# Performance work log

Measured on AMD Instinct MI355X. Metric: run time of the kernel, lower is better.

## Reference

```python
import jax, jax.numpy as jnp
import numpy as np

B = 8192       # atmospheric columns (batch)
NLAY = 60      # vertical levels (RNN sequence length)
NX = 4         # per-level input features
NXS = 3        # surface scalar inputs
NH1 = 64       # rnn1 hidden
NH2 = 64       # rnn2 hidden
NMEM = 16      # latent memory width (nh_mem)
NY = 4         # per-level outputs
NYS = 3        # surface outputs


def _lstm(x, h0, c0, Wih, Whh, bih, bhh):
    """PyTorch-convention LSTM (gate order i,f,g,o). x: [B,T,nx] -> ([B,T,nh], hL, cL)."""
    b = bih + bhh
    WihT = Wih.T
    WhhT = Whh.T

    def step(carry, xt):
        h, c = carry
        g = xt @ WihT + h @ WhhT + b
        i, f, gg, o = jnp.split(g, 4, axis=-1)
        c = jax.nn.sigmoid(f) * c + jax.nn.sigmoid(i) * jnp.tanh(gg)
        h = jax.nn.sigmoid(o) * jnp.tanh(c)
        return (h, c), h

    (hL, cL), ys = jax.lax.scan(step, (h0, c0), jnp.swapaxes(x, 0, 1))
    return jnp.swapaxes(ys, 0, 1), hL, cL


def setup_inputs() -> dict:
    key = jax.random.key(0)
    ks = jax.random.split(key, 30)

    def p(i, shape):
        return jax.random.normal(ks[i], shape, jnp.float32) * 0.05

    return {
        "inputs_main": jax.random.normal(ks[0], (B, NLAY, NX), jnp.float32),
        "inputs_aux": jax.random.normal(ks[1], (B, NXS), jnp.float32),
        "rnn1_mem": jax.random.normal(ks[2], (B, NLAY, NMEM), jnp.float32),
        # mlp_initial: Linear(nx, nneur[0])
        "Wi": p(3, (NH1, NX)), "bi": p(4, (NH1,)),
        # mlp_surface1/2: Linear(nx_sfc, nh_rnn1)
        "Ws1": p(5, (NH1, NXS)), "bs1": p(6, (NH1,)),
        "Ws2": p(7, (NH1, NXS)), "bs2": p(8, (NH1,)),
        # mlp_toa1/2: Linear(1, nh_rnn2)
        "Wt1": p(9, (NH2, 1)), "bt1": p(10, (NH2,)),
        "Wt2": p(11, (NH2, 1)), "bt2": p(12, (NH2,)),
        # rnn1: LSTM(NH1+NMEM -> NH1)
        "Wih1": p(13, (4 * NH1, NH1 + NMEM)), "Whh1": p(14, (4 * NH1, NH1)),
        "bih1": p(15, (4 * NH1,)), "bhh1": p(16, (4 * NH1,)),
        # rnn2: LSTM(NH1 -> NH2)
        "Wih2": p(17, (4 * NH2, NH1)), "Whh2": p(18, (4 * NH2, NH2)),
        "bih2": p(19, (4 * NH2,)), "bhh2": p(20, (4 * NH2,)),
        # mlp_latent: Linear(NH2, NMEM)
        "Wl": p(21, (NMEM, NH2)), "bl": p(22, (NMEM,)),
        # mlp_output: Linear(NMEM, NY)
        "Wo": p(23, (NY, NMEM)), "bo": p(24, (NY,)),
        # mlp_surface_output: Linear(NH2, NYS)
        "Wso": p(25, (NYS, NH2)), "bso": p(26, (NYS,)),
    }


def reference(inputs_main, inputs_aux, rnn1_mem, Wi, bi, Ws1, bs1, Ws2, bs2,
              Wt1, bt1, Wt2, bt2, Wih1, Whh1, bih1, bhh1, Wih2, Whh2, bih2, bhh2,
              Wl, bl, Wo, bo, Wso, bso):
    # initial MLP + tanh
    x = jnp.tanh(inputs_main @ Wi.T + bi)                       # [B,L,NH1]
    # concat convective memory
    x = jnp.concatenate([x, rnn1_mem], axis=2)                  # [B,L,NH1+NMEM]
    # rnn1 runs surface->TOA: flip level axis
    x = jnp.flip(x, axis=1)
    hx = jnp.tanh(inputs_aux @ Ws1.T + bs1)                     # surface-conditioned h0
    cx = jnp.tanh(inputs_aux @ Ws2.T + bs2)
    r1, _, _ = _lstm(x, hx, cx, Wih1, Whh1, bih1, bhh1)
    r1 = jnp.flip(r1, axis=1)                                   # back to TOA->surface
    # rnn2 initialized from TOA scalar
    toa = inputs_aux[:, 1:2]
    hx2 = toa @ Wt1.T + bt1
    cx2 = toa @ Wt2.T + bt2
    r2, hL, _ = _lstm(r1, hx2, cx2, Wih2, Whh2, bih2, bhh2)     # [B,L,NH2]
    # intermediate latent MLP -> new per-level memory
    lat = r2 @ Wl.T + bl                                        # [B,L,NMEM]
    new_mem = lat
    out = lat @ Wo.T + bo                                       # [B,L,NY]
    out_sfc = hL @ Wso.T + bso                                  # [B,NYS]
    return (out, out_sfc, new_mem)
```

## Files before the change

kernel.cpp:

```cpp
#include <hip/hip_runtime.h>
#include <hip/hip_bf16.h>

#define BATCH 8192
#define NLAY  60
#define NH    64
#define ROWS  16
#define TPB   256
#define S1    168
#define S2    136

typedef unsigned short ushort_t;
typedef __attribute__((ext_vector_type(8))) short short8;
typedef __attribute__((ext_vector_type(4))) float f32x4;
typedef __attribute__((ext_vector_type(4))) float f4v;

__device__ __forceinline__ float rcp_(float x) { return __builtin_amdgcn_rcpf(x); }
__device__ __forceinline__ float sigm_(float x) { return rcp_(1.0f + __expf(-x)); }
__device__ __forceinline__ float tanh_(float x) { return 1.0f - 2.0f * rcp_(__expf(2.0f * x) + 1.0f); }
__device__ __forceinline__ ushort_t f2bu(float f) {
  unsigned u = __float_as_uint(f);
  return (ushort_t)((u + 0x7FFFu + ((u >> 16) & 1u)) >> 16);
}
__device__ __forceinline__ unsigned pkbf(float a, float b) {
  union { __hip_bfloat162 h; unsigned u; } c;
  c.h = __float22bfloat162_rn(make_float2(a, b));
  return c.u;
}
__device__ __forceinline__ f32x4 mfma16(short8 a, short8 b, f32x4 c) {
  return __builtin_amdgcn_mfma_f32_16x16x32_bf16(a, b, c, 0, 0, 0);
}

__global__ void wtranspose(const float* __restrict__ Wih1, const float* __restrict__ Whh1,
                           const float* __restrict__ Wih2, const float* __restrict__ Whh2,
                           const float* __restrict__ Wl,   const float* __restrict__ Wo,
                           const float* __restrict__ Wso,  ushort_t* __restrict__ frag) {
  int e = blockIdx.x * 256 + threadIdx.x;
  float v;
  if (e < 40960) {
    int j = e & 7, lx = (e >> 3) & 63, rest = e >> 9;
    int ks = rest % 5, gw = rest / 5;
    int g = gw & 3, wv = gw >> 2;
    int uu = wv * 16 + (lx & 15);
    int k = ks * 32 + (lx >> 4) * 8 + j;
    int row = g * 64 + uu;
    v = (k < 80) ? Wih1[row * 80 + k] : (k < 144 ? Whh1[row * 64 + (k - 80)] : 0.0f);
  } else if (e < 73728) {
    int e2 = e - 40960;
    int j = e2 & 7, lx = (e2 >> 3) & 63, rest = e2 >> 9;
    int ks = rest & 3, g = (rest >> 2) & 3, wv = rest >> 4;
    int uu = wv * 16 + (lx & 15);
    int k = ks * 32 + (lx >> 4) * 8 + j;
    int row = g * 64 + uu;
    v = (k < 64) ? Wih2[row * 64 + k] : Whh2[row * 64 + (k - 64)];
  } else if (e < 74752) {
    int e3 = e - 73728;
    int j = e3 & 7, lx = (e3 >> 3) & 63, ks = e3 >> 9;
    int n = lx & 15, k = ks * 32 + (lx >> 4) * 8 + j;
    v = Wl[n * 64 + k];
  } else if (e < 75776) {
    int e4 = e - 74752;
    int j = e4 & 7, lx = (e4 >> 3) & 63, ks = e4 >> 9;
    int n = lx & 15, k = ks * 32 + (lx >> 4) * 8 + j;
    v = 0.0f;
    if (n < 4) {
#pragma unroll
      for (int m = 0; m < 16; ++m) v += Wo[n * 16 + m] * Wl[m * 64 + k];
    }
  } else {
    int e5 = e - 75776;
    int j = e5 & 7, lx = (e5 >> 3) & 63, ks = e5 >> 9;
    int n = lx & 15, k = ks * 32 + (lx >> 4) * 8 + j;
    v = (n < 3) ? Wso[n * 64 + k] : 0.0f;
  }
  frag[e] = f2bu(v);
}

__global__ __launch_bounds__(TPB, 2)
void lstm_fused(const float* __restrict__ inputs_main, const float* __restrict__ inputs_aux,
                const float* __restrict__ rnn1_mem,
                const float* __restrict__ Wi,  const float* __restrict__ bi,
                const float* __restrict__ Ws1, const float* __restrict__ bs1,
                const float* __restrict__ Ws2, const float* __restrict__ bs2,
                const float* __restrict__ Wt1, const float* __restrict__ bt1,
                const float* __restrict__ Wt2, const float* __restrict__ bt2,
                const float* __restrict__ bih1, const float* __restrict__ bhh1,
                const float* __restrict__ bih2, const float* __restrict__ bhh2,
                const float* __restrict__ bl,  const float* __restrict__ Wo,
                const float* __restrict__ bo,  const float* __restrict__ bso,
                const ushort_t* __restrict__ frag,
                ushort_t* __restrict__ r1buf,
                float* __restrict__ out, float* __restrict__ out_sfc,
                float* __restrict__ new_mem) {
  const ushort_t* W1f = frag;
  const ushort_t* W2f = frag + 40960;
  const ushort_t* WlF = frag + 73728;
  const ushort_t* WcF = frag + 74752;
  const ushort_t* WsF = frag + 75776;

  __shared__ __align__(16) ushort_t xh1[2][16 * S1];
  __shared__ __align__(16) ushort_t xh2[2][16 * S2];
  __shared__ __align__(16) float inmS[16][244];

  const int tid = threadIdx.x;
  const int l  = tid & 63, w = tid >> 6;
  const int ln = l & 15,  lq = l >> 4;
  const int u  = w * 16 + ln;
  const int rowbase = lq * 4;
  const int b0 = blockIdx.x * ROWS;
  const int xr = tid >> 4, xm = tid & 15, xc0 = xm * 4;
  const int rr8 = tid >> 3, ch8 = tid & 7;

  short8 B1f[4][5];
#pragma unroll
  for (int g = 0; g < 4; ++g)
#pragma unroll
    for (int ks = 0; ks < 5; ++ks)
      B1f[g][ks] = *(const short8*)(W1f + (((w * 4 + g) * 5 + ks) << 9) + (l << 3));

  f4v wif[4];
#pragma unroll
  for (int cc = 0; cc < 4; ++cc) wif[cc] = *(const f4v*)(Wi + (xc0 + cc) * 4);
  f4v bifv = *(const f4v*)(bi + xc0);

  float bg1[4];
#pragma unroll
  for (int g = 0; g < 4; ++g) bg1[g] = bih1[g * 64 + u] + bhh1[g * 64 + u];

  for (int e = tid; e < 16 * 240; e += TPB) {
    int r = e / 240, c = e - r * 240;
    inmS[r][c] = inputs_main[(size_t)(b0 + r) * 240 + c];
  }
  {
    int r = tid >> 4, c = 144 + (tid & 15);
    xh1[0][r * S1 + c] = 0; xh1[1][r * S1 + c] = 0;
  }
  __syncthreads();

  float c1[4];
  {
    float mv = rnn1_mem[(size_t)(b0 + xr) * 960 + 59 * 16 + xm];
    xh1[0][xr * S1 + 64 + xm] = f2bu(mv);
    f4v xin = *(const f4v*)&inmS[xr][59 * 4];
    float xp[4];
#pragma unroll
    for (int cc = 0; cc < 4; ++cc)
      xp[cc] = tanh_(bifv[cc] + wif[cc][0]*xin[0] + wif[cc][1]*xin[1] + wif[cc][2]*xin[2] + wif[cc][3]*xin[3]);
    *(uint2*)&xh1[0][xr * S1 + xc0] = make_uint2(pkbf(xp[0], xp[1]), pkbf(xp[2], xp[3]));

    float w10 = Ws1[u * 3 + 0], w11 = Ws1[u * 3 + 1], w12 = Ws1[u * 3 + 2], bb1 = bs1[u];
    float w20 = Ws2[u * 3 + 0], w21 = Ws2[u * 3 + 1], w22 = Ws2[u * 3 + 2], bb2 = bs2[u];
#pragma unroll
    for (int reg = 0; reg < 4; ++reg) {
      int row = rowbase + reg;
      const float* ax = inputs_aux + (size_t)(b0 + row) * 3;
      float a0 = ax[0], a1 = ax[1], a2 = ax[2];
      xh1[0][row * S1 + 80 + u] = f2bu(tanh_(w10 * a0 + w11 * a1 + w12 * a2 + bb1));
      c1[reg] = tanh_(w20 * a0 + w21 * a1 + w22 * a2 + bb2);
    }
  }
  __syncthreads();

  int pb = 0;
  for (int t = NLAY - 1; t >= 0; --t) {
    const int nb = pb ^ 1;
    float mv = 0.0f; f4v xin = {};
    if (t > 0) {
      mv  = rnn1_mem[(size_t)(b0 + xr) * 960 + (t - 1) * 16 + xm];
      xin = *(const f4v*)&inmS[xr][(t - 1) * 4];
    }
    short8 af[5];
#pragma unroll
    for (int ks = 0; ks < 5; ++ks)
      af[ks] = *(const short8*)&xh1[pb][ln * S1 + ks * 32 + lq * 8];

    f32x4 acc[4];
#pragma unroll
    for (int g = 0; g < 4; ++g) acc[g] = (f32x4){bg1[g], bg1[g], bg1[g], bg1[g]};
#pragma unroll
    for (int ks = 0; ks < 5; ++ks)
#pragma unroll
      for (int g = 0; g < 4; ++g) acc[g] = mfma16(af[ks], B1f[g][ks], acc[g]);

    if (t > 0) {
      float xp[4];
#pragma unroll
      for (int cc = 0; cc < 4; ++cc)
        xp[cc] = tanh_(bifv[cc] + wif[cc][0]*xin[0] + wif[cc][1]*xin[1] + wif[cc][2]*xin[2] + wif[cc][3]*xin[3]);
      *(uint2*)&xh1[nb][xr * S1 + xc0] = make_uint2(pkbf(xp[0], xp[1]), pkbf(xp[2], xp[3]));
      xh1[nb][xr * S1 + 64 + xm] = f2bu(mv);
    }

    float h[4];
#pragma unroll
    for (int reg = 0; reg < 4; ++reg) {
      float ig = sigm_(acc[0][reg]);
      float fg = sigm_(acc[1][reg]);
      float gg = tanh_(acc[2][reg]);
      float og = sigm_(acc[3][reg]);
      float c  = fg * c1[reg] + ig * gg;
      c1[reg] = c;
      h[reg] = og * tanh_(c);
    }
    unsigned h01 = pkbf(h[0], h[1]), h23 = pkbf(h[2], h[3]);
    ushort_t hu[4] = {(ushort_t)h01, (ushort_t)(h01 >> 16), (ushort_t)h23, (ushort_t)(h23 >> 16)};
#pragma unroll
    for (int reg = 0; reg < 4; ++reg) {
      r1buf[((size_t)(b0 + rowbase + reg) * 60 + t) * 64 + u] = hu[reg];
      if (t > 0) xh1[nb][(rowbase + reg) * S1 + 80 + u] = hu[reg];
      else       xh2[0][(rowbase + reg) * S2 + u]       = hu[reg];
    }
    __syncthreads();
    pb = nb;
  }

  short8 B2f[4][4];
#pragma unroll
  for (int g = 0; g < 4; ++g)
#pragma unroll
    for (int ks = 0; ks < 4; ++ks)
      B2f[g][ks] = *(const short8*)(W2f + (((w * 4 + g) * 4 + ks) << 9) + (l << 3));
  float bg2[4];
#pragma unroll
  for (int g = 0; g < 4; ++g) bg2[g] = bih2[g * 64 + u] + bhh2[g * 64 + u];

  float c2[4];
  {
    float wt1u = Wt1[u], wt2u = Wt2[u], bt1u = bt1[u], bt2u = bt2[u];
#pragma unroll
    for (int reg = 0; reg < 4; ++reg) {
      int row = rowbase + reg;
      float toa = inputs_aux[(size_t)(b0 + row) * 3 + 1];
      xh2[0][row * S2 + 64 + u] = f2bu(toa * wt1u + bt1u);
      c2[reg] = toa * wt2u + bt2u;
    }
  }
  short8 PW0 = {}, PW1 = {};
  float pbias = 0.0f;
  if (w == 0) {
    PW0 = *(const short8*)(WlF + (l << 3));
    PW1 = *(const short8*)(WlF + 512 + (l << 3));
    pbias = bl[ln];
  } else if (w == 1) {
    PW0 = *(const short8*)(WcF + (l << 3));
    PW1 = *(const short8*)(WcF + 512 + (l << 3));
    if (ln < 4) {
      float a = bo[ln];
#pragma unroll
      for (int m = 0; m < 16; ++m) a += Wo[ln * 16 + m] * bl[m];
      pbias = a;
    }
  } else if (w == 2) {
    PW0 = *(const short8*)(WsF + (l << 3));
    PW1 = *(const short8*)(WsF + 512 + (l << 3));
    pbias = (ln < 3) ? bso[ln] : 0.0f;
  }
  __syncthreads();

  pb = 0;
  for (int t = 0; t < NLAY; ++t) {
    const int nb = pb ^ 1;
    short8 r1v = {};
    if (t < 59 && tid < 128)
      r1v = *(const short8*)(r1buf + ((size_t)(b0 + rr8) * 60 + (t + 1)) * 64 + ch8 * 8);
    short8 af2[4];
#pragma unroll
    for (int ks = 0; ks < 4; ++ks)
      af2[ks] = *(const short8*)&xh2[pb][ln * S2 + ks * 32 + lq * 8];

    f32x4 acc[4];
#pragma unroll
    for (int g = 0; g < 4; ++g) acc[g] = (f32x4){bg2[g], bg2[g], bg2[g], bg2[g]};
#pragma unroll
    for (int ks = 0; ks < 4; ++ks)
#pragma unroll
      for (int g = 0; g < 4; ++g) acc[g] = mfma16(af2[ks], B2f[g][ks], acc[g]);

    if (t > 0 && w < 2) {
      short8 aL0 = *(const short8*)&xh2[pb][ln * S2 + 64 + lq * 8];
      short8 aL1 = *(const short8*)&xh2[pb][ln * S2 + 96 + lq * 8];
      f32x4 ap = (f32x4){pbias, pbias, pbias, pbias};
      ap = mfma16(aL0, PW0, ap);
      ap = mfma16(aL1, PW1, ap);
      if (w == 0) {
#pragma unroll
        for (int reg = 0; reg < 4; ++reg)
          new_mem[((size_t)(b0 + rowbase + reg) * 60 + (t - 1)) * 16 + ln] = ap[reg];
      } else if (ln < 4) {
#pragma unroll
        for (int reg = 0; reg < 4; ++reg)
          out[((size_t)(b0 + rowbase + reg) * 60 + (t - 1)) * 4 + ln] = ap[reg];
      }
    }

    float h[4];
#pragma unroll
    for (int reg = 0; reg < 4; ++reg) {
      float ig = sigm_(acc[0][reg]);
      float fg = sigm_(acc[1][reg]);
      float gg = tanh_(acc[2][reg]);
      float og = sigm_(acc[3][reg]);
      float c  = fg * c2[reg] + ig * gg;
      c2[reg] = c;
      h[reg] = og * tanh_(c);
    }
    unsigned h01 = pkbf(h[0], h[1]), h23 = pkbf(h[2], h[3]);
    ushort_t hu[4] = {(ushort_t)h01, (ushort_t)(h01 >> 16), (ushort_t)h23, (ushort_t)(h23 >> 16)};
#pragma unroll
    for (int reg = 0; reg < 4; ++reg)
      xh2[nb][(rowbase + reg) * S2 + 64 + u] = hu[reg];
    if (t < 59 && tid < 128)
      *(short8*)&xh2[nb][rr8 * S2 + ch8 * 8] = r1v;
    __syncthreads();
    pb = nb;
  }

  if (w < 3) {
    short8 aL0 = *(const short8*)&xh2[0][ln * S2 + 64 + lq * 8];
    short8 aL1 = *(const short8*)&xh2[0][ln * S2 + 96 + lq * 8];
    f32x4 ap = (f32x4){pbias, pbias, pbias, pbias};
    ap = mfma16(aL0, PW0, ap);
    ap = mfma16(aL1, PW1, ap);
    if (w == 0) {
#pragma unroll
      for (int reg = 0; reg < 4; ++reg)
        new_mem[((size_t)(b0 + rowbase + reg) * 60 + 59) * 16 + ln] = ap[reg];
    } else if (w == 1) {
      if (ln < 4) {
#pragma unroll
        for (int reg = 0; reg < 4; ++reg)
          out[((size_t)(b0 + rowbase + reg) * 60 + 59) * 4 + ln] = ap[reg];
      }
    } else {
      if (ln < 3) {
#pragma unroll
        for (int reg = 0; reg < 4; ++reg)
          out_sfc[(size_t)(b0 + rowbase + reg) * 3 + ln] = ap[reg];
      }
    }
  }
}

extern "C" void kernel_launch(void* const* d_in, const int* in_sizes, int n_in,
                              void* d_out, int out_size, void* d_ws, size_t ws_size,
                              hipStream_t stream) {
  (void)in_sizes; (void)n_in; (void)out_size; (void)ws_size;
  const float* inputs_main = (const float*)d_in[0];
  const float* inputs_aux  = (const float*)d_in[1];
  const float* rnn1_mem    = (const float*)d_in[2];
  const float* Wi   = (const float*)d_in[3];
  const float* bi   = (const float*)d_in[4];
  const float* Ws1  = (const float*)d_in[5];
  const float* bs1  = (const float*)d_in[6];
  const float* Ws2  = (const float*)d_in[7];
  const float* bs2  = (const float*)d_in[8];
  const float* Wt1  = (const float*)d_in[9];
  const float* bt1  = (const float*)d_in[10];
  const float* Wt2  = (const float*)d_in[11];
  const float* bt2  = (const float*)d_in[12];
  const float* Wih1 = (const float*)d_in[13];
  const float* Whh1 = (const float*)d_in[14];
  const float* bih1 = (const float*)d_in[15];
  const float* bhh1 = (const float*)d_in[16];
  const float* Wih2 = (const float*)d_in[17];
  const float* Whh2 = (const float*)d_in[18];
  const float* bih2 = (const float*)d_in[19];
  const float* bhh2 = (const float*)d_in[20];
  const float* Wl   = (const float*)d_in[21];
  const float* bl   = (const float*)d_in[22];
  const float* Wo   = (const float*)d_in[23];
  const float* bo   = (const float*)d_in[24];
  const float* Wso  = (const float*)d_in[25];
  const float* bso  = (const float*)d_in[26];

  float* out     = (float*)d_out;
  float* out_sfc = out + (size_t)BATCH * NLAY * 4;
  float* new_mem = out_sfc + (size_t)BATCH * 3;

  ushort_t* frag  = (ushort_t*)d_ws;
  ushort_t* r1buf = (ushort_t*)((char*)d_ws + 153600);

  wtranspose<<<300, 256, 0, stream>>>(Wih1, Whh1, Wih2, Whh2, Wl, Wo, Wso, frag);
  lstm_fused<<<BATCH / ROWS, TPB, 0, stream>>>(
      inputs_main, inputs_aux, rnn1_mem, Wi, bi, Ws1, bs1, Ws2, bs2,
      Wt1, bt1, Wt2, bt2, bih1, bhh1, bih2, bhh2, bl, Wo, bo, bso,
      frag, r1buf, out, out_sfc, new_mem);
}
```

Baseline: 263.5 us.

## Split LSTM gates across 8 waves with shared-memory preactivation exchange

Doubles the block to 512 threads so each wave computes two of the four gate groups. Preactivations are exchanged through shared memory, and each lane then applies the nonlinearities for 2 rows × 1 unit. The memory input and inputs_main are preloaded into LDS as bf16 for the whole sequence, and the double-buffered xh arrays are replaced by single buffers with two barriers per step. The goal is more waves per CU and less per-step MFMA and register load per wave. In exchange it adds an extra barrier and an LDS round-trip on every recurrent step.

```diff
diff --git a/kernel.cpp b/kernel.cpp
--- a/kernel.cpp
+++ b/kernel.cpp
@@ -5,12 +5,15 @@
 #define NLAY  60
 #define NH    64
 #define ROWS  16
-#define TPB   256
-#define S1    168
-#define S2    136
+#define TPB   512
+#define SX    136
+#define SM    968
+#define SP    273
+#define SI    244
 
 typedef unsigned short ushort_t;
 typedef __attribute__((ext_vector_type(8))) short short8;
+typedef __attribute__((ext_vector_type(4))) short short4v;
 typedef __attribute__((ext_vector_type(4))) float f32x4;
 typedef __attribute__((ext_vector_type(4))) float f4v;
 
@@ -21,11 +24,7 @@
   unsigned u = __float_as_uint(f);
   return (ushort_t)((u + 0x7FFFu + ((u >> 16) & 1u)) >> 16);
 }
-__device__ __forceinline__ unsigned pkbf(float a, float b) {
-  union { __hip_bfloat162 h; unsigned u; } c;
-  c.h = __float22bfloat162_rn(make_float2(a, b));
-  return c.u;
-}
+__device__ __forceinline__ float b2fu(ushort_t b) { return __uint_as_float(((unsigned)b) << 16); }
 __device__ __forceinline__ f32x4 mfma16(short8 a, short8 b, f32x4 c) {
   return __builtin_amdgcn_mfma_f32_16x16x32_bf16(a, b, c, 0, 0, 0);
 }
@@ -40,17 +39,18 @@
     int j = e & 7, lx = (e >> 3) & 63, rest = e >> 9;
     int ks = rest % 5, gw = rest / 5;
     int g = gw & 3, wv = gw >> 2;
-    int uu = wv * 16 + (lx & 15);
+    int row = g * 64 + wv * 16 + (lx & 15);
     int k = ks * 32 + (lx >> 4) * 8 + j;
-    int row = g * 64 + uu;
-    v = (k < 80) ? Wih1[row * 80 + k] : (k < 144 ? Whh1[row * 64 + (k - 80)] : 0.0f);
+    v = (k < 64)  ? Wih1[row * 80 + k]
+      : (k < 128) ? Whh1[row * 64 + (k - 64)]
+      : (k < 144) ? Wih1[row * 80 + 64 + (k - 128)]
+      : 0.0f;
   } else if (e < 73728) {
     int e2 = e - 40960;
     int j = e2 & 7, lx = (e2 >> 3) & 63, rest = e2 >> 9;
     int ks = rest & 3, g = (rest >> 2) & 3, wv = rest >> 4;
-    int uu = wv * 16 + (lx & 15);
+    int row = g * 64 + wv * 16 + (lx & 15);
     int k = ks * 32 + (lx >> 4) * 8 + j;
-    int row = g * 64 + uu;
     v = (k < 64) ? Wih2[row * 64 + k] : Whh2[row * 64 + (k - 64)];
   } else if (e < 74752) {
     int e3 = e - 73728;
@@ -75,7 +75,7 @@
   frag[e] = f2bu(v);
 }
 
-__global__ __launch_bounds__(TPB, 2)
+__global__ __launch_bounds__(TPB, 4)
 void lstm_fused(const float* __restrict__ inputs_main, const float* __restrict__ inputs_aux,
                 const float* __restrict__ rnn1_mem,
                 const float* __restrict__ Wi,  const float* __restrict__ bi,
@@ -97,244 +97,276 @@
   const ushort_t* WcF = frag + 74752;
   const ushort_t* WsF = frag + 75776;
 
-  __shared__ __align__(16) ushort_t xh1[2][16 * S1];
-  __shared__ __align__(16) ushort_t xh2[2][16 * S2];
-  __shared__ __align__(16) float inmS[16][244];
-
-  const int tid = threadIdx.x;
-  const int l  = tid & 63, w = tid >> 6;
-  const int ln = l & 15,  lq = l >> 4;
-  const int u  = w * 16 + ln;
-  const int rowbase = lq * 4;
-  const int b0 = blockIdx.x * ROWS;
-  const int xr = tid >> 4, xm = tid & 15, xc0 = xm * 4;
-  const int rr8 = tid >> 3, ch8 = tid & 7;
-
-  short8 B1f[4][5];
-#pragma unroll
-  for (int g = 0; g < 4; ++g)
+  __shared__ __align__(16) ushort_t xh1[16 * SX];
+  __shared__ __align__(16) ushort_t xh2[16 * SX];
+  __shared__ __align__(16) ushort_t memAll[16 * SM];
+  __shared__ __align__(16) float    preactS[16 * SP];
+  __shared__ __align__(16) ushort_t inmB[16 * SI];
+
+  const int tid  = threadIdx.x;
+  const int lane = tid & 63;
+  const int wv   = tid >> 6;
+  const int wq   = wv >> 1;
+  const int gp   = wv & 1;
+  const int ln   = lane & 15;
+  const int lq   = lane >> 4;
+  const int u    = wq * 16 + ln;
+  const int r0   = 2 * wv;
+  const int b0   = blockIdx.x * ROWS;
+
+  short8 Bf[2][5];
+#pragma unroll
+  for (int gi = 0; gi < 2; ++gi) {
+    int g = 2 * gp + gi;
 #pragma unroll
     for (int ks = 0; ks < 5; ++ks)
-      B1f[g][ks] = *(const short8*)(W1f + (((w * 4 + g) * 5 + ks) << 9) + (l << 3));
-
-  f4v wif[4];
-#pragma unroll
-  for (int cc = 0; cc < 4; ++cc) wif[cc] = *(const f4v*)(Wi + (xc0 + cc) * 4);
-  f4v bifv = *(const f4v*)(bi + xc0);
-
-  float bg1[4];
-#pragma unroll
-  for (int g = 0; g < 4; ++g) bg1[g] = bih1[g * 64 + u] + bhh1[g * 64 + u];
+      Bf[gi][ks] = *(const short8*)(W1f + (((wq * 4 + g) * 5 + ks) << 9) + (lane << 3));
+  }
+  float bg[2];
+#pragma unroll
+  for (int gi = 0; gi < 2; ++gi)
+    bg[gi] = bih1[(2 * gp + gi) * 64 + u] + bhh1[(2 * gp + gi) * 64 + u];
+
+  f4v wif = *(const f4v*)(Wi + lane * 4);
+  float bif = bi[lane];
 
   for (int e = tid; e < 16 * 240; e += TPB) {
     int r = e / 240, c = e - r * 240;
-    inmS[r][c] = inputs_main[(size_t)(b0 + r) * 240 + c];
-  }
+    inmB[r * SI + c] = f2bu(inputs_main[(size_t)(b0 + r) * 240 + c]);
+  }
+  for (int e = tid; e < 16 * 960; e += TPB) {
+    int r = e / 960, c = e - r * 960;
+    memAll[r * SM + c] = f2bu(rnn1_mem[(size_t)(b0 + r) * 960 + c]);
+  }
+  __syncthreads();
+
+  float c1[2];
   {
-    int r = tid >> 4, c = 144 + (tid & 15);
-    xh1[0][r * S1 + c] = 0; xh1[1][r * S1 + c] = 0;
-  }
-  __syncthreads();
-
-  float c1[4];
-  {
-    float mv = rnn1_mem[(size_t)(b0 + xr) * 960 + 59 * 16 + xm];
-    xh1[0][xr * S1 + 64 + xm] = f2bu(mv);
-    f4v xin = *(const f4v*)&inmS[xr][59 * 4];
-    float xp[4];
-#pragma unroll
-    for (int cc = 0; cc < 4; ++cc)
-      xp[cc] = tanh_(bifv[cc] + wif[cc][0]*xin[0] + wif[cc][1]*xin[1] + wif[cc][2]*xin[2] + wif[cc][3]*xin[3]);
-    *(uint2*)&xh1[0][xr * S1 + xc0] = make_uint2(pkbf(xp[0], xp[1]), pkbf(xp[2], xp[3]));
-
-    float w10 = Ws1[u * 3 + 0], w11 = Ws1[u * 3 + 1], w12 = Ws1[u * 3 + 2], bb1 = bs1[u];
-    float w20 = Ws2[u * 3 + 0], w21 = Ws2[u * 3 + 1], w22 = Ws2[u * 3 + 2], bb2 = bs2[u];
-#pragma unroll
-    for (int reg = 0; reg < 4; ++reg) {
-      int row = rowbase + reg;
+    float w10 = Ws1[lane * 3 + 0], w11 = Ws1[lane * 3 + 1], w12 = Ws1[lane * 3 + 2], bb1 = bs1[lane];
+    float w20 = Ws2[lane * 3 + 0], w21 = Ws2[lane * 3 + 1], w22 = Ws2[lane * 3 + 2], bb2 = bs2[lane];
+#pragma unroll
+    for (int i = 0; i < 2; ++i) {
+      int row = r0 + i;
       const float* ax = inputs_aux + (size_t)(b0 + row) * 3;
       float a0 = ax[0], a1 = ax[1], a2 = ax[2];
-      xh1[0][row * S1 + 80 + u] = f2bu(tanh_(w10 * a0 + w11 * a1 + w12 * a2 + bb1));
-      c1[reg] = tanh_(w20 * a0 + w21 * a1 + w22 * a2 + bb2);
+      xh1[row * SX + 64 + lane] = f2bu(tanh_(w10 * a0 + w11 * a1 + w12 * a2 + bb1));
+      c1[i] = tanh_(w20 * a0 + w21 * a1 + w22 * a2 + bb2);
+      short4v xi = *(const short4v*)(inmB + row * SI + 59 * 4);
+      float a = bif;
+#pragma unroll
+      for (int c = 0; c < 4; ++c) a += wif[c] * b2fu((ushort_t)xi[c]);
+      xh1[row * SX + lane] = f2bu(tanh_(a));
     }
   }
   __syncthreads();
 
-  int pb = 0;
+  ushort_t* r1w = r1buf + ((size_t)(b0 + r0) * 60 + 59) * 64 + lane;
+
   for (int t = NLAY - 1; t >= 0; --t) {
-    const int nb = pb ^ 1;
-    float mv = 0.0f; f4v xin = {};
+    const ushort_t* xrow = xh1 + ln * SX;
+    short8 af0 = *(const short8*)(xrow + lq * 8);
+    short8 af1 = *(const short8*)(xrow + 32 + lq * 8);
+    short8 af2 = *(const short8*)(xrow + 64 + lq * 8);
+    short8 af3 = *(const short8*)(xrow + 96 + lq * 8);
+    short8 af4 = {};
+    if (lq < 2) af4 = *(const short8*)(memAll + ln * SM + t * 16 + lq * 8);
+
+    f32x4 acc[2];
+#pragma unroll
+    for (int gi = 0; gi < 2; ++gi) acc[gi] = (f32x4){bg[gi], bg[gi], bg[gi], bg[gi]};
+#pragma unroll
+    for (int gi = 0; gi < 2; ++gi) {
+      acc[gi] = mfma16(af0, Bf[gi][0], acc[gi]);
+      acc[gi] = mfma16(af1, Bf[gi][1], acc[gi]);
+      acc[gi] = mfma16(af2, Bf[gi][2], acc[gi]);
+      acc[gi] = mfma16(af3, Bf[gi][3], acc[gi]);
+      acc[gi] = mfma16(af4, Bf[gi][4], acc[gi]);
+    }
+
+    float xg[2];
     if (t > 0) {
-      mv  = rnn1_mem[(size_t)(b0 + xr) * 960 + (t - 1) * 16 + xm];
-      xin = *(const f4v*)&inmS[xr][(t - 1) * 4];
-    }
-    short8 af[5];
-#pragma unroll
-    for (int ks = 0; ks < 5; ++ks)
-      af[ks] = *(const short8*)&xh1[pb][ln * S1 + ks * 32 + lq * 8];
-
-    f32x4 acc[4];
-#pragma unroll
-    for (int g = 0; g < 4; ++g) acc[g] = (f32x4){bg1[g], bg1[g], bg1[g], bg1[g]};
-#pragma unroll
-    for (int ks = 0; ks < 5; ++ks)
-#pragma unroll
-      for (int g = 0; g < 4; ++g) acc[g] = mfma16(af[ks], B1f[g][ks], acc[g]);
-
+#pragma unroll
+      for (int i = 0; i < 2; ++i) {
+        short4v xi = *(const short4v*)(inmB + (r0 + i) * SI + (t - 1) * 4);
+        float a = bif;
+#pragma unroll
+        for (int c = 0; c < 4; ++c) a += wif[c] * b2fu((ushort_t)xi[c]);
+        xg[i] = tanh_(a);
+      }
+    }
+
+#pragma unroll
+    for (int gi = 0; gi < 2; ++gi)
+#pragma unroll
+      for (int reg = 0; reg < 4; ++reg)
+        preactS[(lq * 4 + reg) * SP + (2 * gp + gi) * 68 + u] = acc[gi][reg];
+    __syncthreads();
+
+    float pa[2][4];
+#pragma unroll
+    for (int i = 0; i < 2; ++i)
+#pragma unroll
+      for (int g = 0; g < 4; ++g)
+        pa[i][g] = preactS[(r0 + i) * SP + g * 68 + lane];
+#pragma unroll
+    for (int i = 0; i < 2; ++i) {
+      float ig = sigm_(pa[i][0]);
+      float fg = sigm_(pa[i][1]);
+      float gg = tanh_(pa[i][2]);
+      float og = sigm_(pa[i][3]);
+      float c  = fg * c1[i] + ig * gg;
+      c1[i] = c;
+      ushort_t hu = f2bu(og * tanh_(c));
+      r1w[(size_t)i * 3840] = hu;
+      if (t > 0) xh1[(r0 + i) * SX + 64 + lane] = hu;
+      else       xh2[(r0 + i) * SX + lane]      = hu;
+    }
     if (t > 0) {
-      float xp[4];
-#pragma unroll
-      for (int cc = 0; cc < 4; ++cc)
-        xp[cc] = tanh_(bifv[cc] + wif[cc][0]*xin[0] + wif[cc][1]*xin[1] + wif[cc][2]*xin[2] + wif[cc][3]*xin[3]);
-      *(uint2*)&xh1[nb][xr * S1 + xc0] = make_uint2(pkbf(xp[0], xp[1]), pkbf(xp[2], xp[3]));
-      xh1[nb][xr * S1 + 64 + xm] = f2bu(mv);
-    }
-
-    float h[4];
-#pragma unroll
-    for (int reg = 0; reg < 4; ++reg) {
-      float ig = sigm_(acc[0][reg]);
-      float fg = sigm_(acc[1][reg]);
-      float gg = tanh_(acc[2][reg]);
-      float og = sigm_(acc[3][reg]);
-      float c  = fg * c1[reg] + ig * gg;
-      c1[reg] = c;
-      h[reg] = og * tanh_(c);
-    }
-    unsigned h01 = pkbf(h[0], h[1]), h23 = pkbf(h[2], h[3]);
-    ushort_t hu[4] = {(ushort_t)h01, (ushort_t)(h01 >> 16), (ushort_t)h23, (ushort_t)(h23 >> 16)};
-#pragma unroll
-    for (int reg = 0; reg < 4; ++reg) {
-      r1buf[((size_t)(b0 + rowbase + reg) * 60 + t) * 64 + u] = hu[reg];
-      if (t > 0) xh1[nb][(rowbase + reg) * S1 + 80 + u] = hu[reg];
-      else       xh2[0][(rowbase + reg) * S2 + u]       = hu[reg];
-    }
+      xh1[r0 * SX + lane]       = f2bu(xg[0]);
+      xh1[(r0 + 1) * SX + lane] = f2bu(xg[1]);
+    }
+    r1w -= 64;
     __syncthreads();
-    pb = nb;
-  }
-
-  short8 B2f[4][4];
-#pragma unroll
-  for (int g = 0; g < 4; ++g)
+  }
+
+#pragma unroll
+  for (int gi = 0; gi < 2; ++gi) {
+    int g = 2 * gp + gi;
 #pragma unroll
     for (int ks = 0; ks < 4; ++ks)
-      B2f[g][ks] = *(const short8*)(W2f + (((w * 4 + g) * 4 + ks) << 9) + (l << 3));
-  float bg2[4];
-#pragma unroll
-  for (int g = 0; g < 4; ++g) bg2[g] = bih2[g * 64 + u] + bhh2[g * 64 + u];
-
-  float c2[4];
+      Bf[gi][ks] = *(const short8*)(W2f + (((wq * 4 + g) * 4 + ks) << 9) + (lane << 3));
+  }
+#pragma unroll
+  for (int gi = 0; gi < 2; ++gi)
+    bg[gi] = bih2[(2 * gp + gi) * 64 + u] + bhh2[(2 * gp + gi) * 64 + u];
+
+  float c2[2];
   {
-    float wt1u = Wt1[u], wt2u = Wt2[u], bt1u = bt1[u], bt2u = bt2[u];
-#pragma unroll
-    for (int reg = 0; reg < 4; ++reg) {
-      int row = rowbase + reg;
+    float wt1u = Wt1[lane], wt2u = Wt2[lane], bt1u = bt1[lane], bt2u = bt2[lane];
+#pragma unroll
+    for (int i = 0; i < 2; ++i) {
+      int row = r0 + i;
       float toa = inputs_aux[(size_t)(b0 + row) * 3 + 1];
-      xh2[0][row * S2 + 64 + u] = f2bu(toa * wt1u + bt1u);
-      c2[reg] = toa * wt2u + bt2u;
+      xh2[row * SX + 64 + lane] = f2bu(toa * wt1u + bt1u);
+      c2[i] = toa * wt2u + bt2u;
     }
   }
   short8 PW0 = {}, PW1 = {};
   float pbias = 0.0f;
-  if (w == 0) {
-    PW0 = *(const short8*)(WlF + (l << 3));
-    PW1 = *(const short8*)(WlF + 512 + (l << 3));
+  if (wv == 0) {
+    PW0 = *(const short8*)(WlF + (lane << 3));
+    PW1 = *(const short8*)(WlF + 512 + (lane << 3));
     pbias = bl[ln];
-  } else if (w == 1) {
-    PW0 = *(const short8*)(WcF + (l << 3));
-    PW1 = *(const short8*)(WcF + 512 + (l << 3));
+  } else if (wv == 1) {
+    PW0 = *(const short8*)(WcF + (lane << 3));
+    PW1 = *(const short8*)(WcF + 512 + (lane << 3));
     if (ln < 4) {
       float a = bo[ln];
 #pragma unroll
       for (int m = 0; m < 16; ++m) a += Wo[ln * 16 + m] * bl[m];
       pbias = a;
     }
-  } else if (w == 2) {
-    PW0 = *(const short8*)(WsF + (l << 3));
-    PW1 = *(const short8*)(WsF + 512 + (l << 3));
+  } else if (wv == 2) {
+    PW0 = *(const short8*)(WsF + (lane << 3));
+    PW1 = *(const short8*)(WsF + 512 + (lane << 3));
     pbias = (ln < 3) ? bso[ln] : 0.0f;
   }
+  const ushort_t* r1rp = r1buf + ((size_t)(b0 + r0) * 60 + 1) * 64 + lane;
+  float* nmp = new_mem + (size_t)(b0 + lq * 4) * 960 + ln;
+  float* obp = out + (size_t)(b0 + lq * 4) * 240 + ln;
   __syncthreads();
 
-  pb = 0;
   for (int t = 0; t < NLAY; ++t) {
-    const int nb = pb ^ 1;
-    short8 r1v = {};
-    if (t < 59 && tid < 128)
-      r1v = *(const short8*)(r1buf + ((size_t)(b0 + rr8) * 60 + (t + 1)) * 64 + ch8 * 8);
-    short8 af2[4];
-#pragma unroll
-    for (int ks = 0; ks < 4; ++ks)
-      af2[ks] = *(const short8*)&xh2[pb][ln * S2 + ks * 32 + lq * 8];
-
-    f32x4 acc[4];
-#pragma unroll
-    for (int g = 0; g < 4; ++g) acc[g] = (f32x4){bg2[g], bg2[g], bg2[g], bg2[g]};
-#pragma unroll
-    for (int ks = 0; ks < 4; ++ks)
-#pragma unroll
-      for (int g = 0; g < 4; ++g) acc[g] = mfma16(af2[ks], B2f[g][ks], acc[g]);
-
-    if (t > 0 && w < 2) {
-      short8 aL0 = *(const short8*)&xh2[pb][ln * S2 + 64 + lq * 8];
-      short8 aL1 = *(const short8*)&xh2[pb][ln * S2 + 96 + lq * 8];
+    ushort_t r1a = 0, r1b = 0;
+    if (t < 59) { r1a = r1rp[0]; r1b = r1rp[3840]; }
+
+    const ushort_t* xrow = xh2 + ln * SX;
+    short8 af0 = *(const short8*)(xrow + lq * 8);
+    short8 af1 = *(const short8*)(xrow + 32 + lq * 8);
+    short8 af2 = *(const short8*)(xrow + 64 + lq * 8);
+    short8 af3 = *(const short8*)(xrow + 96 + lq * 8);
+
+    f32x4 acc[2];
+#pragma unroll
+    for (int gi = 0; gi < 2; ++gi) acc[gi] = (f32x4){bg[gi], bg[gi], bg[gi], bg[gi]};
+#pragma unroll
+    for (int gi = 0; gi < 2; ++gi) {
+      acc[gi] = mfma16(af0, Bf[gi][0], acc[gi]);
+      acc[gi] = mfma16(af1, Bf[gi][1], acc[gi]);
+      acc[gi] = mfma16(af2, Bf[gi][2], acc[gi]);
+      acc[gi] = mfma16(af3, Bf[gi][3], acc[gi]);
+    }
+
+    if (t > 0 && wv < 2) {
+      short8 aL0 = *(const short8*)(xrow + 64 + lq * 8);
+      short8 aL1 = *(const short8*)(xrow + 96 + lq * 8);
       f32x4 ap = (f32x4){pbias, pbias, pbias, pbias};
       ap = mfma16(aL0, PW0, ap);
       ap = mfma16(aL1, PW1, ap);
-      if (w == 0) {
-#pragma unroll
-        for (int reg = 0; reg < 4; ++reg)
-          new_mem[((size_t)(b0 + rowbase + reg) * 60 + (t - 1)) * 16 + ln] = ap[reg];
-      } else if (ln < 4) {
-#pragma unroll
-        for (int reg = 0; reg < 4; ++reg)
-          out[((size_t)(b0 + rowbase + reg) * 60 + (t - 1)) * 4 + ln] = ap[reg];
+      if (wv == 0) {
+#pragma unroll
+        for (int reg = 0; reg < 4; ++reg) nmp[reg * 960] = ap[reg];
+        nmp += 16;
+      } else {
+        if (ln < 4) {
+#pragma unroll
+          for (int reg = 0; reg < 4; ++reg) obp[reg * 240] = ap[reg];
+        }
+        obp += 4;
       }
     }
 
-    float h[4];
-#pragma unroll
-    for (int reg = 0; reg < 4; ++reg) {
-      float ig = sigm_(acc[0][reg]);
-      float fg = sigm_(acc[1][reg]);
-      float gg = tanh_(acc[2][reg]);
-      float og = sigm_(acc[3][reg]);
-      float c  = fg * c2[reg] + ig * gg;
-      c2[reg] = c;
-      h[reg] = og * tanh_(c);
-    }
-    unsigned h01 = pkbf(h[0], h[1]), h23 = pkbf(h[2], h[3]);
-    ushort_t hu[4] = {(ushort_t)h01, (ushort_t)(h01 >> 16), (ushort_t)h23, (ushort_t)(h23 >> 16)};
-#pragma unroll
-    for (int reg = 0; reg < 4; ++reg)
-      xh2[nb][(rowbase + reg) * S2 + 64 + u] = hu[reg];
-    if (t < 59 && tid < 128)
-      *(short8*)&xh2[nb][rr8 * S2 + ch8 * 8] = r1v;
+#pragma unroll
+    for (int gi = 0; gi < 2; ++gi)
+#pragma unroll
+      for (int reg = 0; reg < 4; ++reg)
+        preactS[(lq * 4 + reg) * SP + (2 * gp + gi) * 68 + u] = acc[gi][reg];
     __syncthreads();
-    pb = nb;
-  }
-
-  if (w < 3) {
-    short8 aL0 = *(const short8*)&xh2[0][ln * S2 + 64 + lq * 8];
-    short8 aL1 = *(const short8*)&xh2[0][ln * S2 + 96 + lq * 8];
+
+    float pa[2][4];
+#pragma unroll
+    for (int i = 0; i < 2; ++i)
+#pragma unroll
+      for (int g = 0; g < 4; ++g)
+        pa[i][g] = preactS[(r0 + i) * SP + g * 68 + lane];
+#pragma unroll
+    for (int i = 0; i < 2; ++i) {
+      float ig = sigm_(pa[i][0]);
+      float fg = sigm_(pa[i][1]);
+      float gg = tanh_(pa[i][2]);
+      float og = sigm_(pa[i][3]);
+      float c  = fg * c2[i] + ig * gg;
+      c2[i] = c;
+      xh2[(r0 + i) * SX + 64 + lane] = f2bu(og * tanh_(c));
+    }
+    if (t < 59) {
+      xh2[r0 * SX + lane]       = r1a;
+      xh2[(r0 + 1) * SX + lane] = r1b;
+      r1rp += 64;
+    }
+    __syncthreads();
+  }
+
+  if (wv < 3) {
+    const ushort_t* xrow = xh2 + ln * SX;
+    short8 aL0 = *(const short8*)(xrow + 64 + lq * 8);
+    short8 aL1 = *(const short8*)(xrow + 96 + lq * 8);
     f32x4 ap = (f32x4){pbias, pbias, pbias, pbias};
     ap = mfma16(aL0, PW0, ap);
     ap = mfma16(aL1, PW1, ap);
-    if (w == 0) {
-#pragma unroll
-      for (int reg = 0; reg < 4; ++reg)
-        new_mem[((size_t)(b0 + rowbase + reg) * 60 + 59) * 16 + ln] = ap[reg];
-    } else if (w == 1) {
+    if (wv == 0) {
+#pragma unroll
+      for (int reg = 0; reg < 4; ++reg) nmp[reg * 960] = ap[reg];
+    } else if (wv == 1) {
       if (ln < 4) {
 #pragma unroll
-        for (int reg = 0; reg < 4; ++reg)
-          out[((size_t)(b0 + rowbase + reg) * 60 + 59) * 4 + ln] = ap[reg];
+        for (int reg = 0; reg < 4; ++reg) obp[reg * 240] = ap[reg];
       }
     } else {
       if (ln < 3) {
 #pragma unroll
         for (int reg = 0; reg < 4; ++reg)
-          out_sfc[(size_t)(b0 + rowbase + reg) * 3 + ln] = ap[reg];
+          out_sfc[(size_t)(b0 + lq * 4 + reg) * 3 + ln] = ap[reg];
       }
     }
   }
```

New measurement: 284.4 us. 7.9% more time.
